# Kernel optimization log

Hardware: AMD Instinct MI355X
Metric: run time of the kernel (lower is better)

Reference implementation:

```python
import jax, jax.numpy as jnp
import numpy as np

BATCH, IN, HID, OUT = 8192, 784, 4096, 10


def setup_inputs() -> dict:
    key = jax.random.key(0)
    k_x, k_w1, k_b1, k_w2, k_b2 = jax.random.split(key, 5)
    return {
        "x": jax.random.normal(k_x, (BATCH, IN), dtype=jnp.float32),
        "W1": jax.random.normal(k_w1, (HID, IN), dtype=jnp.float32) * 0.05,
        "b1": jax.random.normal(k_b1, (HID,), dtype=jnp.float32) * 0.05,
        "W2": jax.random.normal(k_w2, (OUT, HID), dtype=jnp.float32) * 0.05,
        "b2": jax.random.normal(k_b2, (OUT,), dtype=jnp.float32) * 0.05,
    }


def reference(x, W1, b1, W2, b2):
    # x: [B, 784] -- first layer, so the input is NOT binarized (BNN convention
    # for in_features == 784); only the weight is sign-quantized.
    x = x.reshape(-1, IN)
    Wb1 = jnp.sign(W1)                       # binarized weights in {-1, 0, +1}
    h = jnp.einsum("bi,hi->bh", x, Wb1) + b1  # BinarizeLinear fc1
    h = jnp.clip(h, -1.0, 1.0)               # Hardtanh
    out = jnp.einsum("bh,oh->bo", h, W2) + b2  # plain float fc2
    return out
```

## Files before the change

### kernel.cpp

```cpp
#include <hip/hip_runtime.h>
#include <cstdint>


#define BATCH 8192
#define IN_F  784
#define HID   4096
#define OUT_F 10
#define KP    832
#define NKT   13
#define BM    256
#define BN    256
#define BK    64
#define NCT   (HID / BN)
#define HCS   264

typedef unsigned short u16;
typedef __attribute__((ext_vector_type(4))) unsigned short u16x4;
typedef __attribute__((ext_vector_type(8))) _Float16 f16x8;
typedef __attribute__((ext_vector_type(4))) float    f32x4;

#define BARRIER() do { asm volatile("" ::: "memory"); \
                       __builtin_amdgcn_s_barrier();  \
                       asm volatile("" ::: "memory"); } while (0)
#define WAITV(n)  asm volatile("s_waitcnt vmcnt(" #n ")" ::: "memory")

__device__ __forceinline__ u16 f2h(float f) {
  union { _Float16 h; u16 u; } c;
  c.h = (_Float16)f;
  return c.u;
}

__device__ __forceinline__ void gl_lds16(const void* g, void* l) {
  __builtin_amdgcn_global_load_lds(
      (const __attribute__((address_space(1))) uint32_t*)g,
      (__attribute__((address_space(3))) uint32_t*)l, 16, 0, 0);
}

__global__ void prep_kernel(const float* __restrict__ x, const float* __restrict__ W1,
                            const float* __restrict__ W2,
                            u16* __restrict__ xh, u16* __restrict__ wh,
                            u16* __restrict__ w2h) {
  const int stride = gridDim.x * blockDim.x;
  const int gid = blockIdx.x * blockDim.x + threadIdx.x;
  const int KP4 = KP / 4;
  const int IN4 = IN_F / 4;
  const float4* x4 = (const float4*)x;
  const float4* w4 = (const float4*)W1;
  for (int i = gid; i < BATCH * KP4; i += stride) {
    int b = i / KP4, k = i - b * KP4;
    u16x4 o = {0, 0, 0, 0};
    if (k < IN4) {
      float4 v = x4[(size_t)b * IN4 + k];
      o[0] = f2h(v.x); o[1] = f2h(v.y); o[2] = f2h(v.z); o[3] = f2h(v.w);
    }
    *(u16x4*)&xh[(size_t)b * KP + k * 4] = o;
  }
  for (int i = gid; i < HID * KP4; i += stride) {
    int h = i / KP4, k = i - h * KP4;
    u16x4 o = {0, 0, 0, 0};
    if (k < IN4) {
      float4 v = w4[(size_t)h * IN4 + k];
      o[0] = v.x > 0.f ? 0x3C00 : (v.x < 0.f ? 0xBC00 : 0);
      o[1] = v.y > 0.f ? 0x3C00 : (v.y < 0.f ? 0xBC00 : 0);
      o[2] = v.z > 0.f ? 0x3C00 : (v.z < 0.f ? 0xBC00 : 0);
      o[3] = v.w > 0.f ? 0x3C00 : (v.w < 0.f ? 0xBC00 : 0);
    }
    *(u16x4*)&wh[(size_t)h * KP + k * 4] = o;
  }
  for (int i = gid; i < 16 * HID; i += stride) {
    int o = i >> 12, k = i & (HID - 1);
    w2h[i] = (o < OUT_F) ? f2h(W2[o * HID + k]) : (u16)0;
  }
}

__global__ void __launch_bounds__(512, 2) gemm_kernel(
    const u16* __restrict__ xh, const u16* __restrict__ wh,
    const u16* __restrict__ w2h, const float* __restrict__ b1,
    float* __restrict__ part) {
  __shared__ union {
    struct { u16 A[2][2][128 * BK]; u16 B[2][2][128 * BK]; } m;
    struct { u16 hc[128 * HCS]; u16 w2[16 * 256]; } e;
  } sm;

  const int t   = threadIdx.x;
  const int ct  = blockIdx.x;
  const int br  = blockIdx.y;
  const int w   = t >> 6;
  const int l   = t & 63;
  const int wm  = w >> 2;
  const int wn  = w & 3;
  const int g   = l >> 4;
  const int r16 = l & 15;
  const int swz = (r16 & 7) << 3;

  const int  srow  = t >> 3;
  const int  sslot = (t & 7) ^ (srow & 7);
  const u16* gA = xh + (size_t)(br * BM) * KP + sslot * 8;
  const u16* gB = wh + (size_t)(ct * BN) * KP + sslot * 8;

  auto stA = [&](int tile, int h) {
#pragma unroll
    for (int c = 0; c < 2; ++c)
      gl_lds16(gA + (size_t)(h * 128 + c * 64 + srow) * KP + tile * BK,
               &sm.m.A[tile & 1][h][c * 4096 + t * 8]);
  };
  auto stB = [&](int tile, int h) {
#pragma unroll
    for (int c = 0; c < 2; ++c)
      gl_lds16(gB + (size_t)(h * 128 + c * 64 + srow) * KP + tile * BK,
               &sm.m.B[tile & 1][h][c * 4096 + t * 8]);
  };
  auto rdA = [&](int p, int h, int mi, int kk) -> f16x8 {
    return *(const f16x8*)&sm.m.A[p][h][(mi * 32 + wm * 16 + r16) * BK + ((kk * 32 + g * 8) ^ swz)];
  };
  auto rdB = [&](int p, int h, int ni, int kk) -> f16x8 {
    return *(const f16x8*)&sm.m.B[p][h][(ni * 64 + wn * 16 + r16) * BK + ((kk * 32 + g * 8) ^ swz)];
  };

  f32x4 acc[8][4] = {};

  stA(0, 0); stB(0, 0); stA(0, 1); stB(0, 1);
  WAITV(4);
  BARRIER();

  for (int tt = 0; tt < NKT; ++tt) {
    const int  p    = tt & 1;
    const bool more = (tt + 1 < NKT);
#pragma unroll
    for (int q = 0; q < 4; ++q) {
      const int mh = (q == 1 || q == 2) ? 1 : 0;
      const int nh = q >> 1;
      f16x8 af[4][2], bf[2][2];
#pragma unroll
      for (int ni = 0; ni < 2; ++ni)
#pragma unroll
        for (int kk = 0; kk < 2; ++kk) bf[ni][kk] = rdB(p, nh, ni, kk);
#pragma unroll
      for (int mi = 0; mi < 4; ++mi)
#pragma unroll
        for (int kk = 0; kk < 2; ++kk) af[mi][kk] = rdA(p, mh, mi, kk);
      if (more) {
        if      (q == 0) stA(tt + 1, 0);
        else if (q == 1) stB(tt + 1, 0);
        else if (q == 2) stA(tt + 1, 1);
        else             stB(tt + 1, 1);
        if (q != 2) WAITV(4);
      } else {
        if      (q == 0) WAITV(2);
        else if (q == 1) WAITV(0);
      }
      BARRIER();
      __builtin_amdgcn_s_setprio(1);
#pragma unroll
      for (int kk = 0; kk < 2; ++kk)
#pragma unroll
        for (int mi = 0; mi < 4; ++mi)
#pragma unroll
          for (int ni = 0; ni < 2; ++ni)
            acc[mh * 4 + mi][nh * 2 + ni] = __builtin_amdgcn_mfma_f32_16x16x32_f16(
                af[mi][kk], bf[ni][kk], acc[mh * 4 + mi][nh * 2 + ni], 0, 0, 0);
      __builtin_amdgcn_s_setprio(0);
      if (q == 3) BARRIER();
    }
  }

  {
    int row = t >> 5, sp = t & 31;
    int ls = (sp & 24) | ((sp ^ row) & 7);
    gl_lds16(w2h + (size_t)row * HID + ct * BN + ls * 8, &sm.e.w2[t * 8]);
  }
  float b1v[4];
#pragma unroll
  for (int ni = 0; ni < 4; ++ni) b1v[ni] = b1[ct * BN + ni * 64 + wn * 16 + r16];

  float* partBase = part + ((size_t)ct * BATCH + br * BM) * 16;

#pragma unroll
  for (int p = 0; p < 2; ++p) {
    if (p == 1) BARRIER();
#pragma unroll
    for (int mi = 0; mi < 4; ++mi)
#pragma unroll
      for (int ni = 0; ni < 4; ++ni)
#pragma unroll
        for (int r = 0; r < 4; ++r) {
          float v = acc[p * 4 + mi][ni][r] + b1v[ni];
          v = fminf(fmaxf(v, -1.f), 1.f);
          sm.e.hc[(mi * 32 + wm * 16 + g * 4 + r) * HCS + ni * 64 + wn * 16 + r16] = f2h(v);
        }
    if (p == 0) { WAITV(0); }
    BARRIER();
    f32x4 acc2 = {};
#pragma unroll
    for (int kk = 0; kk < 8; ++kk) {
      f16x8 a2 = *(const f16x8*)&sm.e.hc[(w * 16 + r16) * HCS + kk * 32 + g * 8];
      int s   = kk * 4 + g;
      int sp2 = (s & 24) | ((s ^ r16) & 7);
      f16x8 b2f = *(const f16x8*)&sm.e.w2[r16 * 256 + sp2 * 8];
      acc2 = __builtin_amdgcn_mfma_f32_16x16x32_f16(a2, b2f, acc2, 0, 0, 0);
    }
#pragma unroll
    for (int r = 0; r < 4; ++r)
      partBase[(size_t)(p * 128 + w * 16 + g * 4 + r) * 16 + r16] = acc2[r];
  }
}

__global__ void reduce_kernel(const float* __restrict__ part, const float* __restrict__ b2,
                              float* __restrict__ out) {
  int i = blockIdx.x * blockDim.x + threadIdx.x;
  if (i >= BATCH * OUT_F) return;
  int b = i / OUT_F, o = i - b * OUT_F;
  float acc = b2[o];
#pragma unroll
  for (int c = 0; c < NCT; ++c)
    acc += part[((size_t)c * BATCH + b) * 16 + o];
  out[i] = acc;
}

extern "C" void kernel_launch(void* const* d_in, const int* in_sizes, int n_in,
                              void* d_out, int out_size, void* d_ws, size_t ws_size,
                              hipStream_t stream) {
  const float* x  = (const float*)d_in[0];
  const float* W1 = (const float*)d_in[1];
  const float* b1 = (const float*)d_in[2];
  const float* W2 = (const float*)d_in[3];
  const float* b2 = (const float*)d_in[4];
  float* out = (float*)d_out;

  u16* xh  = (u16*)d_ws;
  u16* wh  = xh + (size_t)BATCH * KP;
  u16* w2h = wh + (size_t)HID * KP;
  float* part = (float*)(w2h + 16 * HID);

  hipLaunchKernelGGL(prep_kernel, dim3(2048), dim3(256), 0, stream, x, W1, W2, xh, wh, w2h);
  hipLaunchKernelGGL(gemm_kernel, dim3(NCT, BATCH / BM), dim3(512), 0, stream,
                     xh, wh, w2h, b1, part);
  hipLaunchKernelGGL(reduce_kernel, dim3((BATCH * OUT_F + 255) / 256), dim3(256), 0, stream,
                     part, b2, out);
}
```

Before: 68.06 us.

## Switch main GEMM to 32x32x16 MFMA with whole-tile staging per K step

Replaces the 16x16x32 MFMA tiling with 32x32x16 MFMA fragments, so each wave holds 4x2 accumulators of 16 floats. The per-quadrant staged loads and barriers are replaced by one stage of the next full A/B tile at the start of each K tile, with a single wait and barrier. This aims to raise MFMA work per LDS fragment read and cut barrier count, with reworked swizzled LDS addressing and a new epilogue row mapping. The risks are less overlap between loads and compute, and different register pressure under the 512-thread, 2-block launch bounds.

```diff
diff --git a/kernel.cpp b/kernel.cpp
--- a/kernel.cpp
+++ b/kernel.cpp
@@ -16,8 +16,9 @@
 
 typedef unsigned short u16;
 typedef __attribute__((ext_vector_type(4))) unsigned short u16x4;
-typedef __attribute__((ext_vector_type(8))) _Float16 f16x8;
-typedef __attribute__((ext_vector_type(4))) float    f32x4;
+typedef __attribute__((ext_vector_type(8)))  _Float16 f16x8;
+typedef __attribute__((ext_vector_type(4)))  float    f32x4;
+typedef __attribute__((ext_vector_type(16))) float    f32x16;
 
 #define BARRIER() do { asm volatile("" ::: "memory"); \
                        __builtin_amdgcn_s_barrier();  \
@@ -78,7 +79,7 @@
     const u16* __restrict__ w2h, const float* __restrict__ b1,
     float* __restrict__ part) {
   __shared__ union {
-    struct { u16 A[2][2][128 * BK]; u16 B[2][2][128 * BK]; } m;
+    struct { u16 A[2][BM * BK]; u16 B[2][BN * BK]; } m;
     struct { u16 hc[128 * HCS]; u16 w2[16 * 256]; } e;
   } sm;
 
@@ -89,78 +90,66 @@
   const int l   = t & 63;
   const int wm  = w >> 2;
   const int wn  = w & 3;
+  const int lo  = l & 31;
+  const int hi  = l >> 5;
   const int g   = l >> 4;
   const int r16 = l & 15;
-  const int swz = (r16 & 7) << 3;
 
   const int  srow  = t >> 3;
   const int  sslot = (t & 7) ^ (srow & 7);
   const u16* gA = xh + (size_t)(br * BM) * KP + sslot * 8;
   const u16* gB = wh + (size_t)(ct * BN) * KP + sslot * 8;
 
-  auto stA = [&](int tile, int h) {
-#pragma unroll
-    for (int c = 0; c < 2; ++c)
-      gl_lds16(gA + (size_t)(h * 128 + c * 64 + srow) * KP + tile * BK,
-               &sm.m.A[tile & 1][h][c * 4096 + t * 8]);
+  auto stage = [&](int tile) {
+    const int b = tile & 1;
+#pragma unroll
+    for (int c = 0; c < 4; ++c)
+      gl_lds16(gA + (size_t)(c * 64 + srow) * KP + tile * BK,
+               &sm.m.A[b][c * 4096 + t * 8]);
+#pragma unroll
+    for (int c = 0; c < 4; ++c)
+      gl_lds16(gB + (size_t)(c * 64 + srow) * KP + tile * BK,
+               &sm.m.B[b][c * 4096 + t * 8]);
   };
-  auto stB = [&](int tile, int h) {
-#pragma unroll
-    for (int c = 0; c < 2; ++c)
-      gl_lds16(gB + (size_t)(h * 128 + c * 64 + srow) * KP + tile * BK,
-               &sm.m.B[tile & 1][h][c * 4096 + t * 8]);
+  auto rdA = [&](int p, int mi, int s) -> f16x8 {
+    int row = mi * 64 + wm * 32 + lo;
+    return *(const f16x8*)&sm.m.A[p][row * 64 + (((s * 2 + hi) ^ (row & 7)) << 3)];
   };
-  auto rdA = [&](int p, int h, int mi, int kk) -> f16x8 {
-    return *(const f16x8*)&sm.m.A[p][h][(mi * 32 + wm * 16 + r16) * BK + ((kk * 32 + g * 8) ^ swz)];
+  auto rdB = [&](int p, int nh, int s) -> f16x8 {
+    int row = nh * 128 + wn * 32 + lo;
+    return *(const f16x8*)&sm.m.B[p][row * 64 + (((s * 2 + hi) ^ (row & 7)) << 3)];
   };
-  auto rdB = [&](int p, int h, int ni, int kk) -> f16x8 {
-    return *(const f16x8*)&sm.m.B[p][h][(ni * 64 + wn * 16 + r16) * BK + ((kk * 32 + g * 8) ^ swz)];
-  };
-
-  f32x4 acc[8][4] = {};
-
-  stA(0, 0); stB(0, 0); stA(0, 1); stB(0, 1);
-  WAITV(4);
-  BARRIER();
+
+  f32x16 acc[4][2] = {};
+
+  stage(0);
 
   for (int tt = 0; tt < NKT; ++tt) {
-    const int  p    = tt & 1;
-    const bool more = (tt + 1 < NKT);
-#pragma unroll
-    for (int q = 0; q < 4; ++q) {
-      const int mh = (q == 1 || q == 2) ? 1 : 0;
-      const int nh = q >> 1;
-      f16x8 af[4][2], bf[2][2];
-#pragma unroll
-      for (int ni = 0; ni < 2; ++ni)
-#pragma unroll
-        for (int kk = 0; kk < 2; ++kk) bf[ni][kk] = rdB(p, nh, ni, kk);
+    const int p = tt & 1;
+#pragma unroll
+    for (int s = 0; s < 4; ++s) {
+      if (s == 0) {
+        if (tt + 1 < NKT) { stage(tt + 1); WAITV(8); }
+        else              { WAITV(0); }
+        BARRIER();
+      }
+      f16x8 af[4], bf[2];
+#pragma unroll
+      for (int nh = 0; nh < 2; ++nh) bf[nh] = rdB(p, nh, s);
+#pragma unroll
+      for (int mi = 0; mi < 4; ++mi) af[mi] = rdA(p, mi, s);
+      if (s == 3) {
+        asm volatile("s_waitcnt lgkmcnt(0)" ::: "memory");
+        __builtin_amdgcn_sched_barrier(0);
+        BARRIER();
+      }
+      __builtin_amdgcn_s_setprio(1);
 #pragma unroll
       for (int mi = 0; mi < 4; ++mi)
 #pragma unroll
-        for (int kk = 0; kk < 2; ++kk) af[mi][kk] = rdA(p, mh, mi, kk);
-      if (more) {
-        if      (q == 0) stA(tt + 1, 0);
-        else if (q == 1) stB(tt + 1, 0);
-        else if (q == 2) stA(tt + 1, 1);
-        else             stB(tt + 1, 1);
-        if (q != 2) WAITV(4);
-      } else {
-        if      (q == 0) WAITV(2);
-        else if (q == 1) WAITV(0);
-      }
-      BARRIER();
-      __builtin_amdgcn_s_setprio(1);
-#pragma unroll
-      for (int kk = 0; kk < 2; ++kk)
-#pragma unroll
-        for (int mi = 0; mi < 4; ++mi)
-#pragma unroll
-          for (int ni = 0; ni < 2; ++ni)
-            acc[mh * 4 + mi][nh * 2 + ni] = __builtin_amdgcn_mfma_f32_16x16x32_f16(
-                af[mi][kk], bf[ni][kk], acc[mh * 4 + mi][nh * 2 + ni], 0, 0, 0);
+        for (int nh = 0; nh < 2; ++nh)
+          acc[mi][nh] = __builtin_amdgcn_mfma_f32_32x32x16_f16(af[mi], bf[nh], acc[mi][nh], 0, 0, 0);
       __builtin_amdgcn_s_setprio(0);
-      if (q == 3) BARRIER();
     }
   }
 
@@ -169,9 +158,9 @@
     int ls = (sp & 24) | ((sp ^ row) & 7);
     gl_lds16(w2h + (size_t)row * HID + ct * BN + ls * 8, &sm.e.w2[t * 8]);
   }
-  float b1v[4];
-#pragma unroll
-  for (int ni = 0; ni < 4; ++ni) b1v[ni] = b1[ct * BN + ni * 64 + wn * 16 + r16];
+  float b1v[2];
+#pragma unroll
+  for (int nh = 0; nh < 2; ++nh) b1v[nh] = b1[ct * BN + nh * 128 + wn * 32 + lo];
 
   float* partBase = part + ((size_t)ct * BATCH + br * BM) * 16;
 
@@ -179,14 +168,15 @@
   for (int p = 0; p < 2; ++p) {
     if (p == 1) BARRIER();
 #pragma unroll
-    for (int mi = 0; mi < 4; ++mi)
-#pragma unroll
-      for (int ni = 0; ni < 4; ++ni)
-#pragma unroll
-        for (int r = 0; r < 4; ++r) {
-          float v = acc[p * 4 + mi][ni][r] + b1v[ni];
+    for (int mi = 0; mi < 2; ++mi)
+#pragma unroll
+      for (int nh = 0; nh < 2; ++nh)
+#pragma unroll
+        for (int r = 0; r < 16; ++r) {
+          float v = acc[p * 2 + mi][nh][r] + b1v[nh];
           v = fminf(fmaxf(v, -1.f), 1.f);
-          sm.e.hc[(mi * 32 + wm * 16 + g * 4 + r) * HCS + ni * 64 + wn * 16 + r16] = f2h(v);
+          int crow = (r & 3) + 8 * (r >> 2) + 4 * hi;
+          sm.e.hc[(mi * 64 + wm * 32 + crow) * HCS + nh * 128 + wn * 32 + lo] = f2h(v);
         }
     if (p == 0) { WAITV(0); }
     BARRIER();
```

Result: slower. 72.24 us (+6.2%).
